# Kernel tuning notes

Measured on AMD Instinct MI355X. Metric: run time of the kernel, lower is better.

The kernel has to match this reference:

```python
import jax, jax.numpy as jnp
import numpy as np


def setup_inputs() -> dict:
    key = jax.random.key(0)
    k1, k2 = jax.random.split(key)
    B, S = 2048, 512
    # effective pixel intensity samples (positive), per pixel over time
    it_eff = jax.random.uniform(k1, (B, S), minval=0.05, maxval=1.05, dtype=jnp.float32)
    # strictly increasing sample timestamps, dt ~ 1e-4 s
    dts = jax.random.uniform(k2, (B, S), minval=5e-5, maxval=1.5e-4, dtype=jnp.float32)
    ts = jnp.cumsum(dts, axis=1)
    return {
        "it_eff": it_eff,
        "ts": ts,
        # buffer (no softplus): tau_in * it_eff product constant
        "tau_in_it_eff_prod": jnp.float32(1e-4),
        # raw (pre-softplus) learned parameters, softplus(raw) = actual value
        "tau_mil_raw": jnp.float32(-9.0),    # tau_mil_it_eff_prod ~ 1.2e-4
        "A_amp_inv_raw": jnp.float32(-3.0),  # A_amp ~ 20.6
        "A_loop_inv_raw": jnp.float32(-4.0), # A_loop ~ 55
        "tau_out_raw": jnp.float32(-8.0),    # tau_out ~ 3.4e-4 s
        "tau_sf_raw": jnp.float32(-9.0),     # tau_sf ~ 1.2e-4 s
        "tau_diff_raw": jnp.float32(-10.0),  # tau_diff ~ 4.5e-5 s
    }


def _forward(it_eff, ts, tau_in_it_eff_prod, tau_mil_raw, A_amp_inv_raw,
             A_loop_inv_raw, tau_out_raw, tau_sf_raw, tau_diff_raw):
    sp = jax.nn.softplus
    tau_mil_prod = sp(tau_mil_raw)
    A_amp = 1.0 / sp(A_amp_inv_raw)
    A_loop = 1.0 / sp(A_loop_inv_raw)
    tau_out = sp(tau_out_raw)
    omega_c_sf = 1.0 / sp(tau_sf_raw)
    omega_c_diff = 1.0 / sp(tau_diff_raw)

    B, S = it_eff.shape
    K = S - 1
    u = jnp.log(it_eff)                      # effective log-intensity input
    dt = ts[:, 1:] - ts[:, :-1]              # [B, K]

    # Linearize NLTI photoreceptor LPF at steady state = next input sample
    I_ss = it_eff[:, 1:]                     # [B, K]
    tau_in = tau_in_it_eff_prod / I_ss
    tau_mil = tau_mil_prod / I_ss
    denom = (tau_in + tau_mil) * tau_out
    two_zeta_omega_n = (tau_in + tau_out + (A_amp + 1.0) * tau_mil) / denom
    omega_n_sq = (A_loop + 1.0) / denom

    # Augmented matrix for FOH discretization: expm([[A*dt, B*dt, 0],[0,0,1],[0,0,0]])
    # top-left -> Ad, col 4 -> Gamma1, col 5 -> Gamma2 (FOH ramp integral / dt)
    em = jnp.zeros((B, K, 6, 6), dtype=it_eff.dtype)
    em = (em.at[..., 0, 0].set(-two_zeta_omega_n * dt)
            .at[..., 0, 1].set(-omega_n_sq * dt)
            .at[..., 1, 0].set(dt)
            .at[..., 2, 1].set(omega_c_sf * dt)
            .at[..., 2, 2].set(-omega_c_sf * dt)
            .at[..., 3, 2].set(omega_c_diff * dt)
            .at[..., 3, 3].set(-omega_c_diff * dt)
            .at[..., 0, 4].set(omega_n_sq * dt)
            .at[..., 4, 5].set(1.0))
    ms = jax.vmap(jax.scipy.linalg.expm)(em.reshape(-1, 6, 6)).reshape(B, K, 6, 6)
    Ad = ms[..., :4, :4]                     # [B, K, 4, 4]
    G1 = ms[..., :4, 4]                      # [B, K, 4]
    G2 = ms[..., :4, 5]                      # [B, K, 4]
    Bd = G1 - G2                             # coeff of u[k]
    Bt = G2                                  # coeff of u[k+1] (FOH)

    # steady-state initial state at u[0]: x = [0, u0, u0, u0]
    u0 = u[:, 0]
    x0 = jnp.stack([jnp.zeros_like(u0), u0, u0, u0], axis=-1)  # [B, 4]

    def step(x, inp):
        Ad_k, Bd_k, Bt_k, u_k, u_k1 = inp
        x_new = (jnp.einsum('bij,bj->bi', Ad_k, x)
                 + Bd_k * u_k[:, None] + Bt_k * u_k1[:, None])
        return x_new, x_new[:, 3]            # diff-amp LPF output state

    xs = (jnp.moveaxis(Ad, 1, 0), jnp.moveaxis(Bd, 1, 0), jnp.moveaxis(Bt, 1, 0),
          u[:, :-1].T, u[:, 1:].T)
    _, ys = jax.lax.scan(step, x0, xs)       # ys: [K, B]
    y = jnp.concatenate([u0[:, None], ys.T], axis=1)  # [B, S]
    return y


def reference(it_eff, ts, tau_in_it_eff_prod, tau_mil_raw, A_amp_inv_raw,
              A_loop_inv_raw, tau_out_raw, tau_sf_raw, tau_diff_raw):
    return _forward(it_eff, ts, tau_in_it_eff_prod, tau_mil_raw, A_amp_inv_raw,
                    A_loop_inv_raw, tau_out_raw, tau_sf_raw, tau_diff_raw)
```

## Files before the change

### kernel.cpp

```cpp
#include <hip/hip_runtime.h>
#include <math.h>

namespace {
constexpr int BB = 2048;
constexpr int SS = 512;
constexpr int NSQ = 4;
constexpr float SCV = 0.0625f;

__device__ __constant__ float INVF[15] = {
    1.0f, 1.0f, 0.5f, 1.66666672e-1f, 4.16666679e-2f, 8.33333377e-3f,
    1.38888892e-3f, 1.98412701e-4f, 2.48015876e-5f, 2.75573195e-6f,
    2.75573188e-7f, 2.50521084e-8f, 2.08767563e-9f, 1.60590438e-10f,
    1.14707456e-11f};
}

struct Aff {
    float a00, a01, a10, a11;
    float a20, a21, a22;
    float a30, a31, a32, a33;
    float c0, c1, c2, c3;
};

__device__ __forceinline__ Aff aff_identity() {
    Aff r;
    r.a00 = 1.f; r.a01 = 0.f; r.a10 = 0.f; r.a11 = 1.f;
    r.a20 = 0.f; r.a21 = 0.f; r.a22 = 1.f;
    r.a30 = 0.f; r.a31 = 0.f; r.a32 = 0.f; r.a33 = 1.f;
    r.c0 = 0.f; r.c1 = 0.f; r.c2 = 0.f; r.c3 = 0.f;
    return r;
}

__device__ __forceinline__ Aff aff_compose(const Aff& s, const Aff& f) {
    Aff r;
    r.a00 = s.a00*f.a00 + s.a01*f.a10;
    r.a01 = s.a00*f.a01 + s.a01*f.a11;
    r.a10 = s.a10*f.a00 + s.a11*f.a10;
    r.a11 = s.a10*f.a01 + s.a11*f.a11;
    r.a20 = s.a20*f.a00 + s.a21*f.a10 + s.a22*f.a20;
    r.a21 = s.a20*f.a01 + s.a21*f.a11 + s.a22*f.a21;
    r.a22 = s.a22*f.a22;
    r.a30 = s.a30*f.a00 + s.a31*f.a10 + s.a32*f.a20 + s.a33*f.a30;
    r.a31 = s.a30*f.a01 + s.a31*f.a11 + s.a32*f.a21 + s.a33*f.a31;
    r.a32 = s.a32*f.a22 + s.a33*f.a32;
    r.a33 = s.a33*f.a33;
    r.c0 = s.a00*f.c0 + s.a01*f.c1 + s.c0;
    r.c1 = s.a10*f.c0 + s.a11*f.c1 + s.c1;
    r.c2 = s.a20*f.c0 + s.a21*f.c1 + s.a22*f.c2 + s.c2;
    r.c3 = s.a30*f.c0 + s.a31*f.c1 + s.a32*f.c2 + s.a33*f.c3 + s.c3;
    return r;
}

__device__ __forceinline__ Aff aff_shfl_up(const Aff& a, int d) {
    Aff r;
    r.a00 = __shfl_up(a.a00, d, 64); r.a01 = __shfl_up(a.a01, d, 64);
    r.a10 = __shfl_up(a.a10, d, 64); r.a11 = __shfl_up(a.a11, d, 64);
    r.a20 = __shfl_up(a.a20, d, 64); r.a21 = __shfl_up(a.a21, d, 64);
    r.a22 = __shfl_up(a.a22, d, 64);
    r.a30 = __shfl_up(a.a30, d, 64); r.a31 = __shfl_up(a.a31, d, 64);
    r.a32 = __shfl_up(a.a32, d, 64); r.a33 = __shfl_up(a.a33, d, 64);
    r.c0 = __shfl_up(a.c0, d, 64); r.c1 = __shfl_up(a.c1, d, 64);
    r.c2 = __shfl_up(a.c2, d, 64); r.c3 = __shfl_up(a.c3, d, 64);
    return r;
}

__device__ __forceinline__ Aff aff_sel_ident(const Aff& p, bool ok) {
    Aff r;
    r.a00 = ok ? p.a00 : 1.f; r.a01 = ok ? p.a01 : 0.f;
    r.a10 = ok ? p.a10 : 0.f; r.a11 = ok ? p.a11 : 1.f;
    r.a20 = ok ? p.a20 : 0.f; r.a21 = ok ? p.a21 : 0.f;
    r.a22 = ok ? p.a22 : 1.f;
    r.a30 = ok ? p.a30 : 0.f; r.a31 = ok ? p.a31 : 0.f;
    r.a32 = ok ? p.a32 : 0.f; r.a33 = ok ? p.a33 : 1.f;
    r.c0 = ok ? p.c0 : 0.f; r.c1 = ok ? p.c1 : 0.f;
    r.c2 = ok ? p.c2 : 0.f; r.c3 = ok ? p.c3 : 0.f;
    return r;
}

__device__ __forceinline__ void aff_apply(const Aff& m, float& x0, float& x1,
                                          float& x2, float& x3) {
    const float y0 = m.a00*x0 + m.a01*x1 + m.c0;
    const float y1 = m.a10*x0 + m.a11*x1 + m.c1;
    const float y2 = m.a20*x0 + m.a21*x1 + m.a22*x2 + m.c2;
    const float y3 = m.a30*x0 + m.a31*x1 + m.a32*x2 + m.a33*x3 + m.c3;
    x0 = y0; x1 = y1; x2 = y2; x3 = y3;
}

__global__ __launch_bounds__(256) void pbw_kernel(
    const float* __restrict__ it_eff,
    const float* __restrict__ ts,
    const float* __restrict__ p_tin_prod,
    const float* __restrict__ p_tmil_raw,
    const float* __restrict__ p_aamp_raw,
    const float* __restrict__ p_aloop_raw,
    const float* __restrict__ p_tout_raw,
    const float* __restrict__ p_tsf_raw,
    const float* __restrict__ p_tdiff_raw,
    float* __restrict__ out)
{
    __shared__ float sc[15 * SS];
    __shared__ float su[SS];
    __shared__ float sy[SS];
    __shared__ float swc[4 * 15];

    const int b = blockIdx.x;
    const int t = threadIdx.x;
    const int lane = t & 63;
    const int wv = t >> 6;

    const float tin_prod  = p_tin_prod[0];
    const float tmil_prod = log1pf(expf(p_tmil_raw[0]));
    const float Aamp1     = 1.0f / log1pf(expf(p_aamp_raw[0])) + 1.0f;
    const float Aloop1    = 1.0f / log1pf(expf(p_aloop_raw[0])) + 1.0f;
    const float tau_out   = log1pf(expf(p_tout_raw[0]));
    const float wsf       = 1.0f / log1pf(expf(p_tsf_raw[0]));
    const float wdf       = 1.0f / log1pf(expf(p_tdiff_raw[0]));

    const float* rowI = it_eff + (size_t)b * SS;
    const float* rowT = ts     + (size_t)b * SS;

    for (int j = t; j < SS; j += 256) su[j] = logf(rowI[j]);
    __syncthreads();

    for (int k = t; k < SS; k += 256) {
        if (k == SS - 1) {
            sc[0*SS+k] = 1.f; sc[1*SS+k] = 0.f; sc[2*SS+k] = 0.f; sc[3*SS+k] = 1.f;
            sc[4*SS+k] = 0.f; sc[5*SS+k] = 0.f; sc[6*SS+k] = 1.f;
            sc[7*SS+k] = 0.f; sc[8*SS+k] = 0.f; sc[9*SS+k] = 0.f; sc[10*SS+k] = 1.f;
            sc[11*SS+k] = 0.f; sc[12*SS+k] = 0.f; sc[13*SS+k] = 0.f; sc[14*SS+k] = 0.f;
            continue;
        }
        const float I  = rowI[k + 1];
        const float dt = rowT[k + 1] - rowT[k];

        const float tin = tin_prod  / I;
        const float tml = tmil_prod / I;
        const float idn = 1.0f / ((tin + tml) * tau_out);
        const float a   = (tin + tau_out + Aamp1 * tml) * idn;
        const float w2  = Aloop1 * idn;
        const float w   = sqrtf(w2);
        const float iw  = 1.0f / w;

        const float dts = dt * SCV;
        const float f00 = -a * dts;
        const float f01 = -w * dts;
        const float f10 =  w * dts;
        const float f21 =  wsf * dts;
        const float f22 = -f21;
        const float f32 =  wdf * dts;
        const float f33 = -f32;
        const float g0  =  f10;

        float t00 = fmaf(f00, 1.0f/12.0f, 1.0f), t01 = f01 * (1.0f/12.0f);
        float t10 = f10 * (1.0f/12.0f),          t11 = 1.0f;
        float c00 = 0.0f, c01 = f21 * (1.0f/12.0f), c10 = 0.0f, c11 = 0.0f;
        float l00 = fmaf(f22, 1.0f/12.0f, 1.0f);
        float l10 = f32 * (1.0f/12.0f);
        float l11 = fmaf(f33, 1.0f/12.0f, 1.0f);
#pragma unroll
        for (int m = 11; m >= 1; --m) {
            const float rm = 1.0f / (float)m;
            const float p00 = f00*t00 + f01*t10;
            const float p01 = f00*t01 + f01*t11;
            const float p10 = f10*t00;
            const float p11 = f10*t01;
            const float q00 = f21*t10 + f22*c00;
            const float q01 = f21*t11 + f22*c01;
            const float q10 = f32*c00 + f33*c10;
            const float q11 = f32*c01 + f33*c11;
            const float m00 = f22*l00;
            const float m10 = f32*l00 + f33*l10;
            const float m11 = f33*l11;
            t00 = fmaf(p00, rm, 1.0f); t01 = p01*rm;
            t10 = p10*rm;              t11 = fmaf(p11, rm, 1.0f);
            c00 = q00*rm; c01 = q01*rm; c10 = q10*rm; c11 = q11*rm;
            l00 = fmaf(m00, rm, 1.0f); l10 = m10*rm; l11 = fmaf(m11, rm, 1.0f);
        }

        float p0 = g0, p1 = 0.0f, p2 = 0.0f, p3 = 0.0f;
        float g10 = 0, g11 = 0, g12 = 0, g13 = 0;
        float g20 = 0, g21 = 0, g22 = 0, g23 = 0;
#pragma unroll
        for (int n = 0; n <= 12; ++n) {
            const float c1 = INVF[n + 1], c2 = INVF[n + 2];
            g10 = fmaf(p0, c1, g10); g11 = fmaf(p1, c1, g11);
            g12 = fmaf(p2, c1, g12); g13 = fmaf(p3, c1, g13);
            g20 = fmaf(p0, c2, g20); g21 = fmaf(p1, c2, g21);
            g22 = fmaf(p2, c2, g22); g23 = fmaf(p3, c2, g23);
            const float np0 = f00*p0 + f01*p1;
            const float np1 = f10*p0;
            const float np2 = f21*p1 + f22*p2;
            const float np3 = f32*p2 + f33*p3;
            p0 = np0; p1 = np1; p2 = np2; p3 = np3;
        }
        g20 *= SCV; g21 *= SCV; g22 *= SCV; g23 *= SCV;
        float h = SCV;

#pragma unroll
        for (int i = 0; i < NSQ; ++i) {
            const float e2v0 = t00*g20 + t01*g21;
            const float e2v1 = t10*g20 + t11*g21;
            const float e2v2 = c00*g20 + c01*g21 + l00*g22;
            const float e2v3 = c10*g20 + c11*g21 + l10*g22 + l11*g23;
            const float e1v0 = t00*g10 + t01*g11;
            const float e1v1 = t10*g10 + t11*g11;
            const float e1v2 = c00*g10 + c01*g11 + l00*g12;
            const float e1v3 = c10*g10 + c11*g11 + l10*g12 + l11*g13;
            g20 = e2v0 + h*g10 + g20; g21 = e2v1 + h*g11 + g21;
            g22 = e2v2 + h*g12 + g22; g23 = e2v3 + h*g13 + g23;
            g10 = e1v0 + g10; g11 = e1v1 + g11;
            g12 = e1v2 + g12; g13 = e1v3 + g13;
            h += h;
            const float p00 = t00*t00 + t01*t10;
            const float p01 = t00*t01 + t01*t11;
            const float p10 = t10*t00 + t11*t10;
            const float p11 = t10*t01 + t11*t11;
            const float q00 = c00*t00 + c01*t10 + l00*c00;
            const float q01 = c00*t01 + c01*t11 + l00*c01;
            const float q10 = c10*t00 + c11*t10 + l10*c00 + l11*c10;
            const float q11 = c10*t01 + c11*t11 + l10*c01 + l11*c11;
            const float m00 = l00*l00;
            const float m10 = l10*l00 + l11*l10;
            const float m11 = l11*l11;
            t00 = p00; t01 = p01; t10 = p10; t11 = p11;
            c00 = q00; c01 = q01; c10 = q10; c11 = q11;
            l00 = m00; l10 = m10; l11 = m11;
        }

        const float a00 = t00,      a01 = w * t01;
        const float a10 = t10 * iw, a11 = t11;
        const float a20 = c00 * iw, a21 = c01, a22 = l00;
        const float a30 = c10 * iw, a31 = c11, a32 = l10, a33 = l11;
        g10 *= w; g20 *= w;
        const float bd0 = g10 - g20, bd1 = g11 - g21;
        const float bd2 = g12 - g22, bd3 = g13 - g23;

        const float uk  = su[k];
        const float uk1 = su[k + 1];

        sc[ 0*SS+k] = a00; sc[ 1*SS+k] = a01; sc[ 2*SS+k] = a10; sc[ 3*SS+k] = a11;
        sc[ 4*SS+k] = a20; sc[ 5*SS+k] = a21; sc[ 6*SS+k] = a22;
        sc[ 7*SS+k] = a30; sc[ 8*SS+k] = a31; sc[ 9*SS+k] = a32; sc[10*SS+k] = a33;
        sc[11*SS+k] = fmaf(bd0, uk, g20 * uk1);
        sc[12*SS+k] = fmaf(bd1, uk, g21 * uk1);
        sc[13*SS+k] = fmaf(bd2, uk, g22 * uk1);
        sc[14*SS+k] = fmaf(bd3, uk, g23 * uk1);
    }

    __syncthreads();

    const int k0 = 2 * t;
    float v1[15], v2[15];
#pragma unroll
    for (int w = 0; w < 15; ++w) {
        const float2 vv = *(const float2*)&sc[w * SS + k0];
        v1[w] = vv.x; v2[w] = vv.y;
    }
    Aff m1, m2;
    m1.a00=v1[0]; m1.a01=v1[1]; m1.a10=v1[2]; m1.a11=v1[3];
    m1.a20=v1[4]; m1.a21=v1[5]; m1.a22=v1[6];
    m1.a30=v1[7]; m1.a31=v1[8]; m1.a32=v1[9]; m1.a33=v1[10];
    m1.c0=v1[11]; m1.c1=v1[12]; m1.c2=v1[13]; m1.c3=v1[14];
    m2.a00=v2[0]; m2.a01=v2[1]; m2.a10=v2[2]; m2.a11=v2[3];
    m2.a20=v2[4]; m2.a21=v2[5]; m2.a22=v2[6];
    m2.a30=v2[7]; m2.a31=v2[8]; m2.a32=v2[9]; m2.a33=v2[10];
    m2.c0=v2[11]; m2.c1=v2[12]; m2.c2=v2[13]; m2.c3=v2[14];

    Aff cur = aff_compose(m2, m1);

#pragma unroll
    for (int d = 1; d < 64; d <<= 1) {
        Aff p = aff_shfl_up(cur, d);
        p = aff_sel_ident(p, lane >= d);
        cur = aff_compose(cur, p);
    }

    if (lane == 63) {
        float* dst = &swc[wv * 15];
        dst[0]=cur.a00; dst[1]=cur.a01; dst[2]=cur.a10; dst[3]=cur.a11;
        dst[4]=cur.a20; dst[5]=cur.a21; dst[6]=cur.a22;
        dst[7]=cur.a30; dst[8]=cur.a31; dst[9]=cur.a32; dst[10]=cur.a33;
        dst[11]=cur.c0; dst[12]=cur.c1; dst[13]=cur.c2; dst[14]=cur.c3;
    }
    __syncthreads();

    const float u0 = su[0];
    float x0 = 0.0f, x1 = u0, x2 = u0, x3 = u0;
    for (int j = 0; j < wv; ++j) {
        const float* m = &swc[j * 15];
        Aff wm;
        wm.a00=m[0]; wm.a01=m[1]; wm.a10=m[2]; wm.a11=m[3];
        wm.a20=m[4]; wm.a21=m[5]; wm.a22=m[6];
        wm.a30=m[7]; wm.a31=m[8]; wm.a32=m[9]; wm.a33=m[10];
        wm.c0=m[11]; wm.c1=m[12]; wm.c2=m[13]; wm.c3=m[14];
        aff_apply(wm, x0, x1, x2, x3);
    }

    Aff ex = aff_shfl_up(cur, 1);
    ex = aff_sel_ident(ex, lane >= 1);
    aff_apply(ex, x0, x1, x2, x3);

    aff_apply(m1, x0, x1, x2, x3);
    sy[k0 + 1] = x3;
    aff_apply(m2, x0, x1, x2, x3);
    if (k0 + 2 < SS) sy[k0 + 2] = x3;
    if (t == 0) sy[0] = u0;

    __syncthreads();

    const int base = b * SS;
    out[base + t]       = sy[t];
    out[base + 256 + t] = sy[256 + t];
}

extern "C" void kernel_launch(void* const* d_in, const int* in_sizes, int n_in,
                              void* d_out, int out_size, void* d_ws, size_t ws_size,
                              hipStream_t stream) {
    const float* it_eff = (const float*)d_in[0];
    const float* ts     = (const float*)d_in[1];
    const float* p2 = (const float*)d_in[2];
    const float* p3 = (const float*)d_in[3];
    const float* p4 = (const float*)d_in[4];
    const float* p5 = (const float*)d_in[5];
    const float* p6 = (const float*)d_in[6];
    const float* p7 = (const float*)d_in[7];
    const float* p8 = (const float*)d_in[8];
    float* out = (float*)d_out;

    pbw_kernel<<<dim3(BB), dim3(256), 0, stream>>>(
        it_eff, ts, p2, p3, p4, p5, p6, p7, p8, out);
}
```

Before: 108.7 us.

## Compute step matrices in registers with lower-order series and fast intrinsics

The kernel drops the 15xSS shared-memory staging buffer, and each thread now builds its two step affine maps directly in registers from global loads. The Taylor series order is cut, from 12 to 6 terms for the exponential and from 13 to 7 for the Gamma series. Division, sqrt and log are replaced with the AMD rcp/rsq/log hardware intrinsics, and the denominator algebra is simplified with precomputed products. This removes most of the per-step ALU work and the shared-memory round trip, but the lower series order and approximate intrinsics reduce accuracy.

```diff
diff --git a/kernel.cpp b/kernel.cpp
--- a/kernel.cpp
+++ b/kernel.cpp
@@ -6,12 +6,12 @@
 constexpr int SS = 512;
 constexpr int NSQ = 4;
 constexpr float SCV = 0.0625f;
-
-__device__ __constant__ float INVF[15] = {
-    1.0f, 1.0f, 0.5f, 1.66666672e-1f, 4.16666679e-2f, 8.33333377e-3f,
-    1.38888892e-3f, 1.98412701e-4f, 2.48015876e-5f, 2.75573195e-6f,
-    2.75573188e-7f, 2.50521084e-8f, 2.08767563e-9f, 1.60590438e-10f,
-    1.14707456e-11f};
+}
+
+__device__ __forceinline__ float frcp(float x) { return __builtin_amdgcn_rcpf(x); }
+__device__ __forceinline__ float frsq(float x) { return __builtin_amdgcn_rsqf(x); }
+__device__ __forceinline__ float flog(float x) {
+    return __builtin_amdgcn_logf(x) * 0.69314718056f;
 }
 
 struct Aff {
@@ -85,6 +85,122 @@
     x0 = y0; x1 = y1; x2 = y2; x3 = y3;
 }
 
+__device__ __forceinline__ Aff make_step(
+    float Iss, float dt, float uk, float uk1,
+    float sprod, float aprod, float tau_out, float Aloop1,
+    float wsf, float wdf)
+{
+    const float rI  = frcp(Iss);
+    const float s   = sprod * rI;
+    const float idn = frcp(s * tau_out);
+    const float a   = fmaf(aprod, rI, tau_out) * idn;
+    const float w2  = Aloop1 * idn;
+    const float iw  = frsq(w2);
+    const float w   = w2 * iw;
+
+    const float dts = dt * SCV;
+    const float f00 = -a * dts;
+    const float f01 = -w * dts;
+    const float f10 =  w * dts;
+    const float f21 =  wsf * dts;
+    const float f22 = -f21;
+    const float f32 =  wdf * dts;
+    const float f33 = -f32;
+    const float g0  =  f10;
+
+    float t00 = fmaf(f00, 1.0f/6.0f, 1.0f), t01 = f01 * (1.0f/6.0f);
+    float t10 = f10 * (1.0f/6.0f),          t11 = 1.0f;
+    float c00 = 0.0f, c01 = f21 * (1.0f/6.0f), c10 = 0.0f, c11 = 0.0f;
+    float l00 = fmaf(f22, 1.0f/6.0f, 1.0f);
+    float l10 = f32 * (1.0f/6.0f);
+    float l11 = fmaf(f33, 1.0f/6.0f, 1.0f);
+#pragma unroll
+    for (int m = 5; m >= 1; --m) {
+        const float rm = 1.0f / (float)m;
+        const float p00 = f00*t00 + f01*t10;
+        const float p01 = f00*t01 + f01*t11;
+        const float p10 = f10*t00;
+        const float p11 = f10*t01;
+        const float q00 = f21*t10 + f22*c00;
+        const float q01 = f21*t11 + f22*c01;
+        const float q10 = f32*c00 + f33*c10;
+        const float q11 = f32*c01 + f33*c11;
+        const float m00 = f22*l00;
+        const float m10 = f32*l00 + f33*l10;
+        const float m11 = f33*l11;
+        t00 = fmaf(p00, rm, 1.0f); t01 = p01*rm;
+        t10 = p10*rm;              t11 = fmaf(p11, rm, 1.0f);
+        c00 = q00*rm; c01 = q01*rm; c10 = q10*rm; c11 = q11*rm;
+        l00 = fmaf(m00, rm, 1.0f); l10 = m10*rm; l11 = fmaf(m11, rm, 1.0f);
+    }
+
+    constexpr float INV[9] = {1.0f, 1.0f, 0.5f, 1.6666667e-1f, 4.1666668e-2f,
+                              8.3333338e-3f, 1.3888889e-3f, 1.9841270e-4f,
+                              2.4801588e-5f};
+    float p0 = g0, p1 = 0.0f, p2 = 0.0f, p3 = 0.0f;
+    float g10 = 0, g11 = 0, g12 = 0, g13 = 0;
+    float g20 = 0, g21 = 0, g22 = 0, g23 = 0;
+#pragma unroll
+    for (int n = 0; n <= 6; ++n) {
+        const float c1 = INV[n + 1], c2 = INV[n + 2];
+        g10 = fmaf(p0, c1, g10); g11 = fmaf(p1, c1, g11);
+        g12 = fmaf(p2, c1, g12); g13 = fmaf(p3, c1, g13);
+        g20 = fmaf(p0, c2, g20); g21 = fmaf(p1, c2, g21);
+        g22 = fmaf(p2, c2, g22); g23 = fmaf(p3, c2, g23);
+        const float np0 = f00*p0 + f01*p1;
+        const float np1 = f10*p0;
+        const float np2 = f21*p1 + f22*p2;
+        const float np3 = f32*p2 + f33*p3;
+        p0 = np0; p1 = np1; p2 = np2; p3 = np3;
+    }
+    g20 *= SCV; g21 *= SCV; g22 *= SCV; g23 *= SCV;
+    float h = SCV;
+
+#pragma unroll
+    for (int i = 0; i < NSQ; ++i) {
+        const float e2v0 = t00*g20 + t01*g21;
+        const float e2v1 = t10*g20 + t11*g21;
+        const float e2v2 = c00*g20 + c01*g21 + l00*g22;
+        const float e2v3 = c10*g20 + c11*g21 + l10*g22 + l11*g23;
+        const float e1v0 = t00*g10 + t01*g11;
+        const float e1v1 = t10*g10 + t11*g11;
+        const float e1v2 = c00*g10 + c01*g11 + l00*g12;
+        const float e1v3 = c10*g10 + c11*g11 + l10*g12 + l11*g13;
+        g20 = e2v0 + h*g10 + g20; g21 = e2v1 + h*g11 + g21;
+        g22 = e2v2 + h*g12 + g22; g23 = e2v3 + h*g13 + g23;
+        g10 = e1v0 + g10; g11 = e1v1 + g11;
+        g12 = e1v2 + g12; g13 = e1v3 + g13;
+        h += h;
+        const float p00 = t00*t00 + t01*t10;
+        const float p01 = t00*t01 + t01*t11;
+        const float p10 = t10*t00 + t11*t10;
+        const float p11 = t10*t01 + t11*t11;
+        const float q00 = c00*t00 + c01*t10 + l00*c00;
+        const float q01 = c00*t01 + c01*t11 + l00*c01;
+        const float q10 = c10*t00 + c11*t10 + l10*c00 + l11*c10;
+        const float q11 = c10*t01 + c11*t11 + l10*c01 + l11*c11;
+        const float m00 = l00*l00;
+        const float m10 = l10*l00 + l11*l10;
+        const float m11 = l11*l11;
+        t00 = p00; t01 = p01; t10 = p10; t11 = p11;
+        c00 = q00; c01 = q01; c10 = q10; c11 = q11;
+        l00 = m00; l10 = m10; l11 = m11;
+    }
+
+    Aff r;
+    r.a00 = t00;      r.a01 = w * t01;
+    r.a10 = t10 * iw; r.a11 = t11;
+    r.a20 = c00 * iw; r.a21 = c01; r.a22 = l00;
+    r.a30 = c10 * iw; r.a31 = c11; r.a32 = l10; r.a33 = l11;
+    g10 *= w; g20 *= w;
+    const float du = uk1 - uk;
+    r.c0 = fmaf(g10, uk, g20 * du);
+    r.c1 = fmaf(g11, uk, g21 * du);
+    r.c2 = fmaf(g12, uk, g22 * du);
+    r.c3 = fmaf(g13, uk, g23 * du);
+    return r;
+}
+
 __global__ __launch_bounds__(256) void pbw_kernel(
     const float* __restrict__ it_eff,
     const float* __restrict__ ts,
@@ -97,10 +213,8 @@
     const float* __restrict__ p_tdiff_raw,
     float* __restrict__ out)
 {
-    __shared__ float sc[15 * SS];
-    __shared__ float su[SS];
+    __shared__ float swc[4 * 15];
     __shared__ float sy[SS];
-    __shared__ float swc[4 * 15];
 
     const int b = blockIdx.x;
     const int t = threadIdx.x;
@@ -114,156 +228,32 @@
     const float tau_out   = log1pf(expf(p_tout_raw[0]));
     const float wsf       = 1.0f / log1pf(expf(p_tsf_raw[0]));
     const float wdf       = 1.0f / log1pf(expf(p_tdiff_raw[0]));
+    const float sprod = tin_prod + tmil_prod;
+    const float aprod = fmaf(Aamp1, tmil_prod, tin_prod);
 
     const float* rowI = it_eff + (size_t)b * SS;
     const float* rowT = ts     + (size_t)b * SS;
 
-    for (int j = t; j < SS; j += 256) su[j] = logf(rowI[j]);
-    __syncthreads();
-
-    for (int k = t; k < SS; k += 256) {
-        if (k == SS - 1) {
-            sc[0*SS+k] = 1.f; sc[1*SS+k] = 0.f; sc[2*SS+k] = 0.f; sc[3*SS+k] = 1.f;
-            sc[4*SS+k] = 0.f; sc[5*SS+k] = 0.f; sc[6*SS+k] = 1.f;
-            sc[7*SS+k] = 0.f; sc[8*SS+k] = 0.f; sc[9*SS+k] = 0.f; sc[10*SS+k] = 1.f;
-            sc[11*SS+k] = 0.f; sc[12*SS+k] = 0.f; sc[13*SS+k] = 0.f; sc[14*SS+k] = 0.f;
-            continue;
-        }
-        const float I  = rowI[k + 1];
-        const float dt = rowT[k + 1] - rowT[k];
-
-        const float tin = tin_prod  / I;
-        const float tml = tmil_prod / I;
-        const float idn = 1.0f / ((tin + tml) * tau_out);
-        const float a   = (tin + tau_out + Aamp1 * tml) * idn;
-        const float w2  = Aloop1 * idn;
-        const float w   = sqrtf(w2);
-        const float iw  = 1.0f / w;
-
-        const float dts = dt * SCV;
-        const float f00 = -a * dts;
-        const float f01 = -w * dts;
-        const float f10 =  w * dts;
-        const float f21 =  wsf * dts;
-        const float f22 = -f21;
-        const float f32 =  wdf * dts;
-        const float f33 = -f32;
-        const float g0  =  f10;
-
-        float t00 = fmaf(f00, 1.0f/12.0f, 1.0f), t01 = f01 * (1.0f/12.0f);
-        float t10 = f10 * (1.0f/12.0f),          t11 = 1.0f;
-        float c00 = 0.0f, c01 = f21 * (1.0f/12.0f), c10 = 0.0f, c11 = 0.0f;
-        float l00 = fmaf(f22, 1.0f/12.0f, 1.0f);
-        float l10 = f32 * (1.0f/12.0f);
-        float l11 = fmaf(f33, 1.0f/12.0f, 1.0f);
-#pragma unroll
-        for (int m = 11; m >= 1; --m) {
-            const float rm = 1.0f / (float)m;
-            const float p00 = f00*t00 + f01*t10;
-            const float p01 = f00*t01 + f01*t11;
-            const float p10 = f10*t00;
-            const float p11 = f10*t01;
-            const float q00 = f21*t10 + f22*c00;
-            const float q01 = f21*t11 + f22*c01;
-            const float q10 = f32*c00 + f33*c10;
-            const float q11 = f32*c01 + f33*c11;
-            const float m00 = f22*l00;
-            const float m10 = f32*l00 + f33*l10;
-            const float m11 = f33*l11;
-            t00 = fmaf(p00, rm, 1.0f); t01 = p01*rm;
-            t10 = p10*rm;              t11 = fmaf(p11, rm, 1.0f);
-            c00 = q00*rm; c01 = q01*rm; c10 = q10*rm; c11 = q11*rm;
-            l00 = fmaf(m00, rm, 1.0f); l10 = m10*rm; l11 = fmaf(m11, rm, 1.0f);
-        }
-
-        float p0 = g0, p1 = 0.0f, p2 = 0.0f, p3 = 0.0f;
-        float g10 = 0, g11 = 0, g12 = 0, g13 = 0;
-        float g20 = 0, g21 = 0, g22 = 0, g23 = 0;
-#pragma unroll
-        for (int n = 0; n <= 12; ++n) {
-            const float c1 = INVF[n + 1], c2 = INVF[n + 2];
-            g10 = fmaf(p0, c1, g10); g11 = fmaf(p1, c1, g11);
-            g12 = fmaf(p2, c1, g12); g13 = fmaf(p3, c1, g13);
-            g20 = fmaf(p0, c2, g20); g21 = fmaf(p1, c2, g21);
-            g22 = fmaf(p2, c2, g22); g23 = fmaf(p3, c2, g23);
-            const float np0 = f00*p0 + f01*p1;
-            const float np1 = f10*p0;
-            const float np2 = f21*p1 + f22*p2;
-            const float np3 = f32*p2 + f33*p3;
-            p0 = np0; p1 = np1; p2 = np2; p3 = np3;
-        }
-        g20 *= SCV; g21 *= SCV; g22 *= SCV; g23 *= SCV;
-        float h = SCV;
-
-#pragma unroll
-        for (int i = 0; i < NSQ; ++i) {
-            const float e2v0 = t00*g20 + t01*g21;
-            const float e2v1 = t10*g20 + t11*g21;
-            const float e2v2 = c00*g20 + c01*g21 + l00*g22;
-            const float e2v3 = c10*g20 + c11*g21 + l10*g22 + l11*g23;
-            const float e1v0 = t00*g10 + t01*g11;
-            const float e1v1 = t10*g10 + t11*g11;
-            const float e1v2 = c00*g10 + c01*g11 + l00*g12;
-            const float e1v3 = c10*g10 + c11*g11 + l10*g12 + l11*g13;
-            g20 = e2v0 + h*g10 + g20; g21 = e2v1 + h*g11 + g21;
-            g22 = e2v2 + h*g12 + g22; g23 = e2v3 + h*g13 + g23;
-            g10 = e1v0 + g10; g11 = e1v1 + g11;
-            g12 = e1v2 + g12; g13 = e1v3 + g13;
-            h += h;
-            const float p00 = t00*t00 + t01*t10;
-            const float p01 = t00*t01 + t01*t11;
-            const float p10 = t10*t00 + t11*t10;
-            const float p11 = t10*t01 + t11*t11;
-            const float q00 = c00*t00 + c01*t10 + l00*c00;
-            const float q01 = c00*t01 + c01*t11 + l00*c01;
-            const float q10 = c10*t00 + c11*t10 + l10*c00 + l11*c10;
-            const float q11 = c10*t01 + c11*t11 + l10*c01 + l11*c11;
-            const float m00 = l00*l00;
-            const float m10 = l10*l00 + l11*l10;
-            const float m11 = l11*l11;
-            t00 = p00; t01 = p01; t10 = p10; t11 = p11;
-            c00 = q00; c01 = q01; c10 = q10; c11 = q11;
-            l00 = m00; l10 = m10; l11 = m11;
-        }
-
-        const float a00 = t00,      a01 = w * t01;
-        const float a10 = t10 * iw, a11 = t11;
-        const float a20 = c00 * iw, a21 = c01, a22 = l00;
-        const float a30 = c10 * iw, a31 = c11, a32 = l10, a33 = l11;
-        g10 *= w; g20 *= w;
-        const float bd0 = g10 - g20, bd1 = g11 - g21;
-        const float bd2 = g12 - g22, bd3 = g13 - g23;
-
-        const float uk  = su[k];
-        const float uk1 = su[k + 1];
-
-        sc[ 0*SS+k] = a00; sc[ 1*SS+k] = a01; sc[ 2*SS+k] = a10; sc[ 3*SS+k] = a11;
-        sc[ 4*SS+k] = a20; sc[ 5*SS+k] = a21; sc[ 6*SS+k] = a22;
-        sc[ 7*SS+k] = a30; sc[ 8*SS+k] = a31; sc[ 9*SS+k] = a32; sc[10*SS+k] = a33;
-        sc[11*SS+k] = fmaf(bd0, uk, g20 * uk1);
-        sc[12*SS+k] = fmaf(bd1, uk, g21 * uk1);
-        sc[13*SS+k] = fmaf(bd2, uk, g22 * uk1);
-        sc[14*SS+k] = fmaf(bd3, uk, g23 * uk1);
-    }
-
-    __syncthreads();
-
     const int k0 = 2 * t;
-    float v1[15], v2[15];
-#pragma unroll
-    for (int w = 0; w < 15; ++w) {
-        const float2 vv = *(const float2*)&sc[w * SS + k0];
-        v1[w] = vv.x; v2[w] = vv.y;
-    }
-    Aff m1, m2;
-    m1.a00=v1[0]; m1.a01=v1[1]; m1.a10=v1[2]; m1.a11=v1[3];
-    m1.a20=v1[4]; m1.a21=v1[5]; m1.a22=v1[6];
-    m1.a30=v1[7]; m1.a31=v1[8]; m1.a32=v1[9]; m1.a33=v1[10];
-    m1.c0=v1[11]; m1.c1=v1[12]; m1.c2=v1[13]; m1.c3=v1[14];
-    m2.a00=v2[0]; m2.a01=v2[1]; m2.a10=v2[2]; m2.a11=v2[3];
-    m2.a20=v2[4]; m2.a21=v2[5]; m2.a22=v2[6];
-    m2.a30=v2[7]; m2.a31=v2[8]; m2.a32=v2[9]; m2.a33=v2[10];
-    m2.c0=v2[11]; m2.c1=v2[12]; m2.c2=v2[13]; m2.c3=v2[14];
+    const float2 I01 = *(const float2*)(rowI + k0);
+    const float2 T01 = *(const float2*)(rowT + k0);
+    const bool has2 = (k0 + 2 < SS);
+    const float I2 = has2 ? rowI[k0 + 2] : 1.0f;
+    const float T2 = has2 ? rowT[k0 + 2] : (T01.y + 1e-4f);
+    const float uk0 = flog(I01.x);
+    const float uk1 = flog(I01.y);
+    const float uk2 = flog(I2);
+    const float u0  = flog(rowI[0]);
+
+    Aff m1 = make_step(I01.y, T01.y - T01.x, uk0, uk1,
+                       sprod, aprod, tau_out, Aloop1, wsf, wdf);
+    Aff m2;
+    if (has2) {
+        m2 = make_step(I2, T2 - T01.y, uk1, uk2,
+                       sprod, aprod, tau_out, Aloop1, wsf, wdf);
+    } else {
+        m2 = aff_identity();
+    }
 
     Aff cur = aff_compose(m2, m1);
 
@@ -283,7 +273,6 @@
     }
     __syncthreads();
 
-    const float u0 = su[0];
     float x0 = 0.0f, x1 = u0, x2 = u0, x3 = u0;
     for (int j = 0; j < wv; ++j) {
         const float* m = &swc[j * 15];
@@ -301,8 +290,10 @@
 
     aff_apply(m1, x0, x1, x2, x3);
     sy[k0 + 1] = x3;
-    aff_apply(m2, x0, x1, x2, x3);
-    if (k0 + 2 < SS) sy[k0 + 2] = x3;
+    if (has2) {
+        aff_apply(m2, x0, x1, x2, x3);
+        sy[k0 + 2] = x3;
+    }
     if (t == 0) sy[0] = u0;
 
     __syncthreads();
```

Measured after the change: 103.1 us. 5.1% less time.
